# Optimization experiments

Measured on AMD Instinct MI355X. Metric: run time of the kernel, lower is better.

The kernel has to match this reference:

```python
import jax, jax.numpy as jnp
from jax import lax
import numpy as np

B, T, F = 32, 8192, 16
HID = 128
OUT = 24
K1 = 10


def setup_inputs() -> dict:
    key = jax.random.key(0)
    ks = jax.random.split(key, 5)
    x = jax.random.normal(ks[0], (B, T, F), dtype=jnp.float32)
    # Conv1d(F -> HID, kernel=10): weight (O, I, K), bias (O,)
    w1 = jax.random.normal(ks[1], (HID, F, K1), dtype=jnp.float32) * (1.0 / np.sqrt(F * K1))
    b1 = jax.random.normal(ks[2], (HID,), dtype=jnp.float32) * 0.01
    # Linear(HID*10 -> OUT): weight (OUT, HID*10), bias (OUT,)
    wf = jax.random.normal(ks[3], (OUT, HID * K1), dtype=jnp.float32) * (1.0 / np.sqrt(HID * K1))
    bf = jax.random.normal(ks[4], (OUT,), dtype=jnp.float32) * 0.01
    return {"x": x, "w1": w1, "b1": b1, "wf": wf, "bf": bf}


def reference(x, w1, b1, wf, bf):
    # x: (B, T, F) -> (B, F, T)
    xc = jnp.transpose(x, (0, 2, 1))
    # Conv1d k=10, pad=9 -> length T+9
    h = lax.conv_general_dilated(
        xc, w1, window_strides=(1,), padding=[(9, 9)],
        dimension_numbers=("NCH", "OIH", "NCH")) + b1[None, :, None]  # (B, HID, T+9)
    # out[:, :x.shape[2], :] keeps the first T timesteps
    h = h[:, :, :x.shape[1]]
    h = jnp.concatenate([jnp.repeat(h[:, :, :1], 9, axis=2), h], axis=2)
    # Per-step Linear over flattened 10-step windows == valid conv with k=10.
    # flatten order of window (10, C) is time-major: col index = t*C + c
    kf = jnp.transpose(wf.reshape(wf.shape[0], K1, -1), (0, 2, 1))  # (OUT, HID, 10)
    y = lax.conv_general_dilated(
        h, kf, window_strides=(1,), padding="VALID",
        dimension_numbers=("NCH", "OIH", "NCH")) + bf[None, :, None]  # (B, OUT, T)
    return jnp.transpose(y, (0, 2, 1))  # (B, T, OUT)
```

## Files before the change

kernel.cpp:

```cpp
#include <hip/hip_runtime.h>

#define B_   32
#define T_   8192
#define F_   16
#define OUT_ 24
#define K1_  10
#define ND   19
#define JP   32
#define PADL 24
#define XROWS_TOT (PADL + T_ + 8)
#define TB   512
#define WROWS 536

#define WS_BC_OFF   20480
#define WS_E_OFF    20576
#define WS_W1T_OFF  144992
#define WS_XLO_OFF  226944
#define WS_XHI_OFF  (WS_XLO_OFF + B_ * XROWS_TOT * 8 * 2)

typedef short short8 __attribute__((ext_vector_type(8)));
typedef float float4v __attribute__((ext_vector_type(4)));

__device__ __forceinline__ unsigned short f2bf(float f) {
    unsigned u = __builtin_bit_cast(unsigned, f);
    unsigned r = (u + 0x7fffu + ((u >> 16) & 1u)) >> 16;
    return (unsigned short)r;
}

__device__ __forceinline__ short8 cvt8(float4 f0, float4 f1) {
    short8 v;
    v[0] = (short)f2bf(f0.x); v[1] = (short)f2bf(f0.y);
    v[2] = (short)f2bf(f0.z); v[3] = (short)f2bf(f0.w);
    v[4] = (short)f2bf(f1.x); v[5] = (short)f2bf(f1.y);
    v[6] = (short)f2bf(f1.z); v[7] = (short)f2bf(f1.w);
    return v;
}

__global__ __launch_bounds__(256) void pre_kernel(const float* __restrict__ x,
                                                  const float* __restrict__ w1,
                                                  unsigned short* __restrict__ xlo,
                                                  unsigned short* __restrict__ xhi,
                                                  float* __restrict__ w1t,
                                                  unsigned short* __restrict__ w2pk) {
    int bx = blockIdx.x;
    int tid = threadIdx.x;
    if (bx < 1028) {
        int id = bx * 256 + tid;
        if (id >= B_ * XROWS_TOT) return;
        int b = id / XROWS_TOT, r = id - b * XROWS_TOT;
        int t = r - PADL;
        short8 v0 = short8{0,0,0,0,0,0,0,0}, v1 = v0;
        if (t >= 0 && t < T_) {
            const float4* p = (const float4*)(x + ((long)b * T_ + t) * 16);
            float4 f0 = p[0], f1 = p[1], f2 = p[2], f3 = p[3];
            v0 = cvt8(f0, f1);
            v1 = cvt8(f2, f3);
        }
        *(short8*)(xlo + (size_t)id * 8) = v0;
        *(short8*)(xhi + (size_t)id * 8) = v1;
    } else if (bx < 1108) {
        int idx = (bx - 1028) * 256 + tid;
        float v = w1[idx];
        int c = idx / 160;
        int rem = idx - c * 160;
        int i = rem / 10;
        int k = rem - i * 10;
        w1t[(k * 16 + i) * 128 + c] = v;
    } else {
        int idx = (bx - 1108) * 256 + tid;
        ((unsigned*)w2pk)[idx] = 0;
    }
}

__global__ __launch_bounds__(256) void prep_kernel(const float* __restrict__ w1t,
                                                   const float* __restrict__ b1,
                                                   const float* __restrict__ wf,
                                                   const float* __restrict__ bf,
                                                   unsigned short* __restrict__ w2pk,
                                                   float* __restrict__ bcg,
                                                   float* __restrict__ Eg) {
    int tid = threadIdx.x;
    int lane = tid & 63;
    int wid = blockIdx.x * 4 + (tid >> 6);

    if (wid < 456) {
        int j = wid / ND, d = wid % ND;
        float p[16];
#pragma unroll
        for (int i = 0; i < 16; ++i) p[i] = 0.f;
        int klo = d - 9 > 0 ? d - 9 : 0;
        int khi = d < 9 ? d : 9;
        for (int k = klo; k <= khi; ++k) {
            float w0 = wf[j * 1280 + k * 128 + lane];
            float w1v = wf[j * 1280 + k * 128 + 64 + lane];
            const float* wb = w1t + (d - k) * 16 * 128;
#pragma unroll
            for (int i = 0; i < 16; ++i)
                p[i] = fmaf(w0, wb[i * 128 + lane], fmaf(w1v, wb[i * 128 + 64 + lane], p[i]));
        }
#pragma unroll
        for (int i = 0; i < 16; ++i) {
            p[i] += __shfl_xor(p[i], 1);
            p[i] += __shfl_xor(p[i], 2);
            p[i] += __shfl_xor(p[i], 4);
            p[i] += __shfl_xor(p[i], 8);
            p[i] += __shfl_xor(p[i], 16);
            p[i] += __shfl_xor(p[i], 32);
        }
        if (lane < 16) {
            float v = p[0];
#pragma unroll
            for (int i = 1; i < 16; ++i)
                if (lane == i) v = p[i];
            int kk = d * 16 + lane;
            int ks = kk >> 5, r = kk & 31;
            int quad = r >> 3, z = r & 7;
            int tbl = j >> 4, jj = j & 15;
            int lt = jj + quad * 16;
            w2pk[((tbl * 10 + ks) * 64 + lt) * 8 + z] = f2bf(v);
        }
    } else if (wid < 480) {
        int j = wid - 456;
        float s0 = 0.f, s1 = 0.f;
#pragma unroll
        for (int k = 0; k < K1_; ++k) {
            s0 += wf[j * 1280 + k * 128 + lane];
            s1 += wf[j * 1280 + k * 128 + 64 + lane];
        }
        float s = s0 * b1[lane] + s1 * b1[64 + lane];
        s += __shfl_xor(s, 1);
        s += __shfl_xor(s, 2);
        s += __shfl_xor(s, 4);
        s += __shfl_xor(s, 8);
        s += __shfl_xor(s, 16);
        s += __shfl_xor(s, 32);
        if (lane == 0) bcg[j] = bf[j] + s;
    } else {
        int eidx = wid - 480;
        int t = eidx / 216;
        int rem = eidx % 216;
        int j = rem / 9, tau = rem % 9;
        float p[16];
#pragma unroll
        for (int i = 0; i < 16; ++i) p[i] = 0.f;
        for (int k = 0; k < K1_; ++k) {
            int u = t + k - 9; if (u < 0) u = 0;
            if (tau > u) continue;
            int kap = tau + 9 - u;
            float w0 = wf[j * 1280 + k * 128 + lane];
            float w1v = wf[j * 1280 + k * 128 + 64 + lane];
            const float* wb = w1t + kap * 16 * 128;
#pragma unroll
            for (int i = 0; i < 16; ++i)
                p[i] = fmaf(w0, wb[i * 128 + lane], fmaf(w1v, wb[i * 128 + 64 + lane], p[i]));
        }
#pragma unroll
        for (int i = 0; i < 16; ++i) {
            p[i] += __shfl_xor(p[i], 1);
            p[i] += __shfl_xor(p[i], 2);
            p[i] += __shfl_xor(p[i], 4);
            p[i] += __shfl_xor(p[i], 8);
            p[i] += __shfl_xor(p[i], 16);
            p[i] += __shfl_xor(p[i], 32);
        }
        if (lane < 16) {
            float v = p[0];
#pragma unroll
            for (int i = 1; i < 16; ++i)
                if (lane == i) v = p[i];
            Eg[((t * OUT_ + j) * 9 + tau) * 16 + lane] = v;
        }
    }
}

__global__ __launch_bounds__(256, 2) void main_kernel(const unsigned short* __restrict__ xlo,
                                                      const unsigned short* __restrict__ xhi,
                                                      const unsigned short* __restrict__ w2pk,
                                                      const float* __restrict__ bcg,
                                                      float* __restrict__ out,
                                                      const float* __restrict__ x,
                                                      const float* __restrict__ Eg) {
    int tid = threadIdx.x;
    int b = blockIdx.y;

    if (blockIdx.x == 16) {
        if (tid >= 9 * OUT_) return;
        int t = tid / OUT_, j = tid % OUT_;
        const float4* xv = (const float4*)(x + (long)b * T_ * F_);
        const float4* ev = (const float4*)(Eg + (long)tid * 144);
        float ax = 0.f, ay = 0.f, az = 0.f, aw = 0.f;
#pragma unroll
        for (int q = 0; q < 36; ++q) {
            float4 e = ev[q];
            float4 v = xv[q];
            ax = fmaf(e.x, v.x, ax);
            ay = fmaf(e.y, v.y, ay);
            az = fmaf(e.z, v.z, az);
            aw = fmaf(e.w, v.w, aw);
        }
        out[((long)b * T_ + t) * OUT_ + j] = bcg[j] + ((ax + ay) + (az + aw));
        return;
    }

    __shared__ short xls[2 * WROWS * 8];
    int t0 = blockIdx.x * TB;
    int gbase = PADL + t0 - 18;

    for (int idx = tid; idx < 2 * WROWS; idx += 256) {
        int h = idx >= WROWS;
        int row = h ? idx - WROWS : idx;
        const unsigned short* src = (h ? xhi : xlo) + ((size_t)b * XROWS_TOT + gbase + row) * 8;
        short8 v = *(const short8*)src;
        *(short8*)(xls + (h * WROWS + row) * 8) = v;
    }

    int lane = tid & 63, w = tid >> 6;
    int t = lane & 15, q = lane >> 4;
    int h = q & 1, qh = q >> 1;

    const unsigned short* pk0 = w2pk + lane * 8;
    const unsigned short* pk1 = w2pk + 5120 + lane * 8;
    short8 W0[10], W1[10];
#pragma unroll
    for (int ks = 0; ks < 10; ++ks) {
        W0[ks] = *(const short8*)(pk0 + ks * 512);
        W1[ks] = *(const short8*)(pk1 + ks * 512);
    }

    __syncthreads();

    const short* ap = xls + (h * WROWS + w * 128 + t + qh) * 8;

    float4v acc[8][2];
#pragma unroll
    for (int mt = 0; mt < 8; ++mt) {
        acc[mt][0] = float4v{0.f, 0.f, 0.f, 0.f};
        acc[mt][1] = float4v{0.f, 0.f, 0.f, 0.f};
    }

#pragma unroll
    for (int ks = 0; ks < 10; ++ks) {
#pragma unroll
        for (int mt = 0; mt < 8; ++mt) {
            short8 xf = *(const short8*)(ap + (mt * 16 + 2 * ks) * 8);
            acc[mt][0] = __builtin_amdgcn_mfma_f32_16x16x32_bf16(W0[ks], xf, acc[mt][0], 0, 0, 0);
            acc[mt][1] = __builtin_amdgcn_mfma_f32_16x16x32_bf16(W1[ks], xf, acc[mt][1], 0, 0, 0);
        }
    }

    long outb = (long)b * T_;
    float4 bc0 = *(const float4*)(bcg + q * 4);
    float4 bc1 = (q < 2) ? *(const float4*)(bcg + 16 + q * 4) : make_float4(0.f, 0.f, 0.f, 0.f);
    bool edge = (blockIdx.x == 0);
#pragma unroll
    for (int mt = 0; mt < 8; ++mt) {
        int t_out = t0 + w * 128 + mt * 16 + t;
        if (!edge || t_out >= 9) {
            float* o = out + (outb + t_out) * OUT_;
            float4 v0 = make_float4(acc[mt][0][0] + bc0.x, acc[mt][0][1] + bc0.y,
                                    acc[mt][0][2] + bc0.z, acc[mt][0][3] + bc0.w);
            *(float4*)(o + q * 4) = v0;
            if (q < 2) {
                float4 v1 = make_float4(acc[mt][1][0] + bc1.x, acc[mt][1][1] + bc1.y,
                                        acc[mt][1][2] + bc1.z, acc[mt][1][3] + bc1.w);
                *(float4*)(o + 16 + q * 4) = v1;
            }
        }
    }
}

extern "C" void kernel_launch(void* const* d_in, const int* in_sizes, int n_in,
                              void* d_out, int out_size, void* d_ws, size_t ws_size,
                              hipStream_t stream) {
    const float* x  = (const float*)d_in[0];
    const float* w1 = (const float*)d_in[1];
    const float* b1 = (const float*)d_in[2];
    const float* wf = (const float*)d_in[3];
    const float* bf = (const float*)d_in[4];
    float* out = (float*)d_out;
    unsigned short* w2pk = (unsigned short*)d_ws;
    float* bcg = (float*)((char*)d_ws + WS_BC_OFF);
    float* Eg  = (float*)((char*)d_ws + WS_E_OFF);
    float* w1t = (float*)((char*)d_ws + WS_W1T_OFF);
    unsigned short* xlo = (unsigned short*)((char*)d_ws + WS_XLO_OFF);
    unsigned short* xhi = (unsigned short*)((char*)d_ws + WS_XHI_OFF);

    hipLaunchKernelGGL(pre_kernel, dim3(1148), dim3(256), 0, stream,
                       x, w1, xlo, xhi, w1t, w2pk);
    hipLaunchKernelGGL(prep_kernel, dim3(606), dim3(256), 0, stream,
                       w1t, b1, wf, bf, w2pk, bcg, Eg);
    hipLaunchKernelGGL(main_kernel, dim3(17, B_), dim3(256), 0, stream,
                       xlo, xhi, w2pk, bcg, out, x, Eg);
}
```

Measured before the change: 99.32 us.

## Fuse x bf16 conversion into main kernel, dropping the padded xlo/xhi staging buffers

```diff
diff --git a/kernel.cpp b/kernel.cpp
--- a/kernel.cpp
+++ b/kernel.cpp
@@ -7,16 +7,13 @@
 #define K1_  10
 #define ND   19
 #define JP   32
-#define PADL 24
-#define XROWS_TOT (PADL + T_ + 8)
 #define TB   512
 #define WROWS 536
+#define H1OFF (WROWS * 8 + 8)
 
 #define WS_BC_OFF   20480
 #define WS_E_OFF    20576
 #define WS_W1T_OFF  144992
-#define WS_XLO_OFF  226944
-#define WS_XHI_OFF  (WS_XLO_OFF + B_ * XROWS_TOT * 8 * 2)
 
 typedef short short8 __attribute__((ext_vector_type(8)));
 typedef float float4v __attribute__((ext_vector_type(4)));
@@ -36,30 +33,13 @@
     return v;
 }
 
-__global__ __launch_bounds__(256) void pre_kernel(const float* __restrict__ x,
-                                                  const float* __restrict__ w1,
-                                                  unsigned short* __restrict__ xlo,
-                                                  unsigned short* __restrict__ xhi,
+__global__ __launch_bounds__(256) void pre_kernel(const float* __restrict__ w1,
                                                   float* __restrict__ w1t,
                                                   unsigned short* __restrict__ w2pk) {
     int bx = blockIdx.x;
     int tid = threadIdx.x;
-    if (bx < 1028) {
-        int id = bx * 256 + tid;
-        if (id >= B_ * XROWS_TOT) return;
-        int b = id / XROWS_TOT, r = id - b * XROWS_TOT;
-        int t = r - PADL;
-        short8 v0 = short8{0,0,0,0,0,0,0,0}, v1 = v0;
-        if (t >= 0 && t < T_) {
-            const float4* p = (const float4*)(x + ((long)b * T_ + t) * 16);
-            float4 f0 = p[0], f1 = p[1], f2 = p[2], f3 = p[3];
-            v0 = cvt8(f0, f1);
-            v1 = cvt8(f2, f3);
-        }
-        *(short8*)(xlo + (size_t)id * 8) = v0;
-        *(short8*)(xhi + (size_t)id * 8) = v1;
-    } else if (bx < 1108) {
-        int idx = (bx - 1028) * 256 + tid;
+    if (bx < 80) {
+        int idx = bx * 256 + tid;
         float v = w1[idx];
         int c = idx / 160;
         int rem = idx - c * 160;
@@ -67,7 +47,7 @@
         int k = rem - i * 10;
         w1t[(k * 16 + i) * 128 + c] = v;
     } else {
-        int idx = (bx - 1108) * 256 + tid;
+        int idx = (bx - 80) * 256 + tid;
         ((unsigned*)w2pk)[idx] = 0;
     }
 }
@@ -173,13 +153,11 @@
     }
 }
 
-__global__ __launch_bounds__(256, 2) void main_kernel(const unsigned short* __restrict__ xlo,
-                                                      const unsigned short* __restrict__ xhi,
-                                                      const unsigned short* __restrict__ w2pk,
-                                                      const float* __restrict__ bcg,
-                                                      float* __restrict__ out,
-                                                      const float* __restrict__ x,
-                                                      const float* __restrict__ Eg) {
+__global__ __launch_bounds__(256) void main_kernel(const float* __restrict__ x,
+                                                   const unsigned short* __restrict__ w2pk,
+                                                   const float* __restrict__ bcg,
+                                                   float* __restrict__ out,
+                                                   const float* __restrict__ Eg) {
     int tid = threadIdx.x;
     int b = blockIdx.y;
 
@@ -202,16 +180,19 @@
         return;
     }
 
-    __shared__ short xls[2 * WROWS * 8];
+    __shared__ short xls[2 * WROWS * 8 + 8];
     int t0 = blockIdx.x * TB;
-    int gbase = PADL + t0 - 18;
 
     for (int idx = tid; idx < 2 * WROWS; idx += 256) {
         int h = idx >= WROWS;
         int row = h ? idx - WROWS : idx;
-        const unsigned short* src = (h ? xhi : xlo) + ((size_t)b * XROWS_TOT + gbase + row) * 8;
-        short8 v = *(const short8*)src;
-        *(short8*)(xls + (h * WROWS + row) * 8) = v;
+        int t = t0 - 18 + row;
+        short8 v = short8{0, 0, 0, 0, 0, 0, 0, 0};
+        if (t >= 0 && t < T_) {
+            const float4* p = (const float4*)(x + ((long)b * T_ + t) * 16 + h * 8);
+            v = cvt8(p[0], p[1]);
+        }
+        *(short8*)(xls + h * H1OFF + row * 8) = v;
     }
 
     int lane = tid & 63, w = tid >> 6;
@@ -229,7 +210,7 @@
 
     __syncthreads();
 
-    const short* ap = xls + (h * WROWS + w * 128 + t + qh) * 8;
+    const short* ap = xls + h * H1OFF + (w * 128 + t + qh) * 8;
 
     float4v acc[8][2];
 #pragma unroll
@@ -282,13 +263,10 @@
     float* bcg = (float*)((char*)d_ws + WS_BC_OFF);
     float* Eg  = (float*)((char*)d_ws + WS_E_OFF);
     float* w1t = (float*)((char*)d_ws + WS_W1T_OFF);
-    unsigned short* xlo = (unsigned short*)((char*)d_ws + WS_XLO_OFF);
-    unsigned short* xhi = (unsigned short*)((char*)d_ws + WS_XHI_OFF);
-
-    hipLaunchKernelGGL(pre_kernel, dim3(1148), dim3(256), 0, stream,
-                       x, w1, xlo, xhi, w1t, w2pk);
+
+    hipLaunchKernelGGL(pre_kernel, dim3(120), dim3(256), 0, stream, w1, w1t, w2pk);
     hipLaunchKernelGGL(prep_kernel, dim3(606), dim3(256), 0, stream,
                        w1t, b1, wf, bf, w2pk, bcg, Eg);
     hipLaunchKernelGGL(main_kernel, dim3(17, B_), dim3(256), 0, stream,
-                       xlo, xhi, w2pk, bcg, out, x, Eg);
-}
+                       x, w2pk, bcg, out, Eg);
+}
```

Result: no change. 98.58 us (median of 2 runs) (-0.7%).
